# Performance work log

Measured on AMD Instinct MI355X. Metric: run time of the kernel, lower is better.

## Reference

```python
import jax, jax.numpy as jnp
import numpy as np

ROPE_THETA = 10000.0


def _rotate_half(x):
    # interleaved rotation: out[..., 2i] = -x[..., 2i+1], out[..., 2i+1] = x[..., 2i]
    x_even = x[..., ::2]
    x_odd = x[..., 1::2]
    return jnp.stack([-x_odd, x_even], axis=-1).reshape(x.shape)


def _rope_cos_sin(N, D, dtype):
    inv_freq = 1.0 / (ROPE_THETA ** (jnp.arange(0, D, 2, dtype=jnp.float32) / D))  # [D/2]
    angles = jnp.arange(N, dtype=jnp.float32)[:, None] * inv_freq[None, :]          # [N, D/2]
    angles = jnp.repeat(angles, 2, axis=-1)                                          # [N, D]
    cos = jnp.cos(angles).astype(dtype)[None, :, None, :]  # [1, N, 1, D]
    sin = jnp.sin(angles).astype(dtype)[None, :, None, :]
    return cos, sin


def setup_inputs() -> dict:
    key = jax.random.key(0)
    kq, kk, kv, km = jax.random.split(key, 4)
    B, N, H, D = 16, 1024, 8, 64
    xq = jax.random.normal(kq, (B, N, H, D), dtype=jnp.float32)
    xk = jax.random.normal(kk, (B, N, H, D), dtype=jnp.float32)
    xv = jax.random.normal(kv, (B, N, H, D), dtype=jnp.float32)
    vis_mask = jax.random.bernoulli(km, 0.8, (B, N))  # bool visibility mask per batch
    return {"xq": xq, "xk": xk, "xv": xv, "vis_mask": vis_mask}


def reference(xq, xk, xv, vis_mask):
    B, N, H, D = xq.shape
    sm_scale = 1.0 / np.sqrt(D).astype(np.float32)

    # RoPE (interleaved) on q and k
    cos, sin = _rope_cos_sin(N, D, xq.dtype)
    q = xq * cos + _rotate_half(xq) * sin
    k = xk * cos + _rotate_half(xk) * sin

    # masked full attention: scores [B, H, N, N]
    scores = jnp.einsum("bnhd,bmhd->bhnm", q, k) * sm_scale
    attn_mask = (vis_mask[:, None, :, None] & vis_mask[:, None, None, :])  # [B,1,N,N]
    scores = jnp.where(attn_mask, scores, -jnp.inf)
    p = jax.nn.softmax(scores, axis=-1)
    p = jnp.nan_to_num(p, nan=0.0)  # fully-masked rows -> zeros (matches fallback)
    out = jnp.einsum("bhnm,bmhd->bnhd", p, xv)
    return out
```

## Files before the change

### kernel.cpp

```cpp
#include <hip/hip_runtime.h>
#include <hip/hip_bf16.h>
#include <stdint.h>

#define Bb 16
#define Nn 1024
#define Hh 8
#define Dd 64

typedef unsigned short u16;
typedef float f32x4 __attribute__((ext_vector_type(4)));
typedef short short8 __attribute__((ext_vector_type(8)));

union U4S8 { uint4 u; short8 s; };
union BF2U { __hip_bfloat162 h; uint32_t u; };

__device__ __forceinline__ uint32_t f2bf(float f){
  union{float f;uint32_t i;} v; v.f=f;
  return (v.i + 0x7fffu + ((v.i>>16)&1u))>>16;
}

__device__ __forceinline__ f32x4 mfma16(short8 a, short8 b, f32x4 c){
  return __builtin_amdgcn_mfma_f32_16x16x32_bf16(a,b,c,0,0,0);
}

typedef __attribute__((address_space(3))) uint32_t lds_u32;
typedef const __attribute__((address_space(1))) uint32_t glb_u32;
__device__ __forceinline__ void gl_lds16(const u16* g, u16* l){
  __builtin_amdgcn_global_load_lds((glb_u32*)g, (lds_u32*)l, 16, 0, 0);
}

#define ROPE_K 0.41524101186092030f
#define QS 0.18033688011112042f
#define NEGBIG -1.0e30f

__global__ __launch_bounds__(256) void prepass_kernel(
    const float* __restrict__ xk, const float* __restrict__ xv,
    u16* __restrict__ Kf, u16* __restrict__ Vf)
{
  const int tid = threadIdx.x;
  const int bid = blockIdx.x;
  const int nt = bid & 15, h = (bid>>4)&7, b = bid>>7;
  const size_t bh = (size_t)b*Hh + h;
  const size_t tile = (bh<<4) + nt;

  {
    int r = tid>>2, c = (tid&3)<<4;
    int n = (nt<<6) + r;
    const float4* g = (const float4*)(xk + ((((size_t)b*Nn + n)*Hh + h)<<6) + c);
    float4 a0=g[0],a1=g[1],a2=g[2],a3=g[3];
    float xx[16] = {a0.x,a0.y,a0.z,a0.w, a1.x,a1.y,a1.z,a1.w,
                    a2.x,a2.y,a2.z,a2.w, a3.x,a3.y,a3.z,a3.w};
    uint32_t w[8];
    #pragma unroll
    for (int j=0;j<8;++j){
      int i = (c>>1)+j;
      float inv = exp2f(-(float)i * ROPE_K);
      float ang = (float)n * inv;
      float sn, cs; sincosf(ang, &sn, &cs);
      float x0 = xx[2*j], x1 = xx[2*j+1];
      float q0 = x0*cs - x1*sn;
      float q1 = x1*cs + x0*sn;
      w[j] = f2bf(q0) | (f2bf(q1)<<16);
    }
    int kb = r>>4, l15 = r&15;
    int half = c>>5, qd = (c>>3)&3;
    u16* base = Kf + (tile<<12);
    int dest0 = (kb<<10) + (half<<9) + (qd<<7) + (l15<<3);
    *(uint4*)(base + dest0)       = make_uint4(w[0],w[1],w[2],w[3]);
    *(uint4*)(base + dest0 + 128) = make_uint4(w[4],w[5],w[6],w[7]);
  }

  {
    int k = tid&63, ds = (tid>>6)<<4;
    int n = (nt<<6) + k;
    int slot = (k&1) | (((k>>4)&3)<<1) | (((k>>2)&3)<<3) | (((k>>1)&1)<<5);
    int half = slot>>5, qd = (slot>>3)&3, j = slot&7;
    const float4* g = (const float4*)(xv + ((((size_t)b*Nn + n)*Hh + h)<<6) + ds);
    float4 a0=g[0],a1=g[1],a2=g[2],a3=g[3];
    float vv[16] = {a0.x,a0.y,a0.z,a0.w, a1.x,a1.y,a1.z,a1.w,
                    a2.x,a2.y,a2.z,a2.w, a3.x,a3.y,a3.z,a3.w};
    u16* base = Vf + (tile<<12);
    #pragma unroll
    for (int jj=0;jj<16;++jj){
      int d = ds + jj;
      int s = d>>4, l15v = d&15;
      base[(s<<10) + (half<<9) + (qd<<7) + (l15v<<3) + j] = (u16)f2bf(vv[jj]);
    }
  }
}

__global__ __launch_bounds__(256,2) void attn8_kernel(
    const float* __restrict__ xq, const u16* __restrict__ Kf,
    const u16* __restrict__ Vf, const int* __restrict__ vis,
    float* __restrict__ out)
{
  __shared__ u16 KV[2][2][4096];

  const int tid  = threadIdx.x;
  const int lane = tid & 63;
  const int wave = tid >> 6;
  const int l15  = lane & 15;
  const int quad = lane >> 4;

  const int bid = blockIdx.x;
  const int xcd = bid & 7;
  const int i   = bid >> 3;
  const int bh_ = (xcd<<4) | (i>>2);
  const int qt  = i & 3;
  const int h   = bh_ & 7;
  const int b   = bh_ >> 3;
  const size_t bh = (size_t)bh_;
  const int qbase = qt<<8;

  const int* visb = vis + b*Nn;
  const u16* Kfb = Kf + (bh<<16);
  const u16* Vfb = Vf + (bh<<16);

  short8 qa[4][2];
  #pragma unroll
  for (int mb=0; mb<4; ++mb){
    int n = qbase + (wave<<6) + (mb<<4) + l15;
    const float* src = xq + ((((size_t)b*Nn + n)*Hh + h)<<6);
    #pragma unroll
    for (int half=0; half<2; ++half){
      int d0 = (half<<5) + (quad<<3);
      const float4* g = (const float4*)(src + d0);
      float4 u0 = g[0], u1 = g[1];
      float xx[8] = {u0.x,u0.y,u0.z,u0.w, u1.x,u1.y,u1.z,u1.w};
      uint32_t w[4];
      #pragma unroll
      for (int j=0;j<4;++j){
        int i2 = (d0>>1) + j;
        float inv = exp2f(-(float)i2 * ROPE_K);
        float ang = (float)n * inv;
        float sn, cs; sincosf(ang, &sn, &cs);
        float x0 = xx[2*j], x1 = xx[2*j+1];
        float q0 = (x0*cs - x1*sn)*QS;
        float q1 = (x1*cs + x0*sn)*QS;
        w[j] = f2bf(q0) | (f2bf(q1)<<16);
      }
      U4S8 t; t.u = make_uint4(w[0],w[1],w[2],w[3]);
      qa[mb][half] = t.s;
    }
  }

  U4S8 ones_u; ones_u.u = make_uint4(0x3F803F80u,0x3F803F80u,0x3F803F80u,0x3F803F80u);
  const short8 ones = ones_u.s;

  f32x4 acc[4][4];
  f32x4 l_acc[4];
  #pragma unroll
  for (int mb=0;mb<4;++mb){
    l_acc[mb] = (f32x4){0.f,0.f,0.f,0.f};
    #pragma unroll
    for (int s=0;s<4;++s) acc[mb][s] = (f32x4){0.f,0.f,0.f,0.f};
  }

  const int t8 = tid<<3;

  gl_lds16(Kfb + t8,        &KV[0][0][t8]);
  gl_lds16(Kfb + 2048 + t8, &KV[0][0][2048 + t8]);
  gl_lds16(Vfb + t8,        &KV[0][1][t8]);
  gl_lds16(Vfb + 2048 + t8, &KV[0][1][2048 + t8]);
  __syncthreads();

  for (int kt=0; kt<16; ++kt){
    const int cur = kt & 1;
    if (kt < 15){
      const u16* kg = Kfb + ((kt+1)<<12);
      const u16* vg = Vfb + ((kt+1)<<12);
      gl_lds16(kg + t8,        &KV[cur^1][0][t8]);
      gl_lds16(kg + 2048 + t8, &KV[cur^1][0][2048 + t8]);
      gl_lds16(vg + t8,        &KV[cur^1][1][t8]);
      gl_lds16(vg + 2048 + t8, &KV[cur^1][1][2048 + t8]);
    }

    uint32_t pk[4][2][4];
    #pragma unroll
    for (int kb=0;kb<4;++kb){
      short8 kf0 = *(const short8*)&KV[cur][0][(kb<<10) + (lane<<3)];
      short8 kf1 = *(const short8*)&KV[cur][0][(kb<<10) + 512 + (lane<<3)];
      int4 vi = *(const int4*)&visb[(kt<<6)+(kb<<4)+(quad<<2)];
      f32x4 bias;
      bias.x = vi.x ? 0.f : NEGBIG;
      bias.y = vi.y ? 0.f : NEGBIG;
      bias.z = vi.z ? 0.f : NEGBIG;
      bias.w = vi.w ? 0.f : NEGBIG;
      #pragma unroll
      for (int mb=0;mb<4;++mb){
        f32x4 t = mfma16(kf0, qa[mb][0], bias);
        t = mfma16(kf1, qa[mb][1], t);
        float p0 = __builtin_amdgcn_exp2f(t.x);
        float p1 = __builtin_amdgcn_exp2f(t.y);
        float p2 = __builtin_amdgcn_exp2f(t.z);
        float p3 = __builtin_amdgcn_exp2f(t.w);
        BF2U e0; e0.h = __float22bfloat162_rn(make_float2(p0,p1));
        BF2U e1; e1.h = __float22bfloat162_rn(make_float2(p2,p3));
        pk[kb][0][mb] = e0.u;
        pk[kb][1][mb] = e1.u;
      }
    }

    short8 pa[4][2];
    #pragma unroll
    for (int mb=0;mb<4;++mb){
      U4S8 a0; a0.u = make_uint4(pk[0][0][mb], pk[1][0][mb], pk[2][0][mb], pk[3][0][mb]);
      U4S8 a1; a1.u = make_uint4(pk[0][1][mb], pk[1][1][mb], pk[2][1][mb], pk[3][1][mb]);
      pa[mb][0] = a0.s; pa[mb][1] = a1.s;
    }

    #pragma unroll
    for (int mb=0;mb<4;++mb){
      l_acc[mb] = mfma16(pa[mb][0], ones, l_acc[mb]);
      l_acc[mb] = mfma16(pa[mb][1], ones, l_acc[mb]);
    }
    #pragma unroll
    for (int s=0;s<4;++s){
      short8 vb0 = *(const short8*)&KV[cur][1][(s<<10) + (lane<<3)];
      short8 vb1 = *(const short8*)&KV[cur][1][(s<<10) + 512 + (lane<<3)];
      #pragma unroll
      for (int mb=0;mb<4;++mb){
        acc[mb][s] = mfma16(pa[mb][0], vb0, acc[mb][s]);
        acc[mb][s] = mfma16(pa[mb][1], vb1, acc[mb][s]);
      }
    }

    __syncthreads();
  }

  #pragma unroll
  for (int mb=0;mb<4;++mb){
    int4 qvi = *(const int4*)&visb[qbase + (wave<<6) + (mb<<4) + (quad<<2)];
    int qv[4] = {qvi.x, qvi.y, qvi.z, qvi.w};
    #pragma unroll
    for (int rr=0;rr<4;++rr){
      float lq = l_acc[mb][rr];
      float invl = (qv[rr] != 0 && lq > 0.f) ? 1.f/lq : 0.f;
      int qrow = qbase + (wave<<6) + (mb<<4) + (quad<<2) + rr;
      float* ob = out + ((((size_t)b*Nn + qrow)*Hh + h)<<6);
      #pragma unroll
      for (int s=0;s<4;++s)
        ob[(s<<4)+l15] = acc[mb][s][rr]*invl;
    }
  }
}

__device__ __forceinline__ void stage_rope_row_fb(const float* __restrict__ src,
                                                  u16 (*dst)[72],
                                                  int n_global, int sr, int d0)
{
  const float4* g = (const float4*)src;
  float4 a0 = g[0], a1 = g[1], a2 = g[2], a3 = g[3];
  float xx[16] = {a0.x,a0.y,a0.z,a0.w, a1.x,a1.y,a1.z,a1.w,
                  a2.x,a2.y,a2.z,a2.w, a3.x,a3.y,a3.z,a3.w};
  uint32_t w[8];
  #pragma unroll
  for (int j=0;j<8;++j){
    int i = (d0>>1)+j;
    float inv = exp2f(-(float)i * ROPE_K);
    float ang = (float)n_global * inv;
    float sn, cs; sincosf(ang, &sn, &cs);
    float x0 = xx[2*j], x1 = xx[2*j+1];
    float q0 = x0*cs - x1*sn;
    float q1 = x1*cs + x0*sn;
    w[j] = f2bf(q0) | (f2bf(q1)<<16);
  }
  *(uint4*)&dst[sr][d0]   = make_uint4(w[0],w[1],w[2],w[3]);
  *(uint4*)&dst[sr][d0+8] = make_uint4(w[4],w[5],w[6],w[7]);
}

__global__ __launch_bounds__(256,2) void attn_fallback(
    const float* __restrict__ xq, const float* __restrict__ xk,
    const float* __restrict__ xv, const int* __restrict__ vis,
    float* __restrict__ out)
{
  __shared__ u16 Qs[64][72];
  __shared__ u16 Ks[64][72];
  __shared__ u16 Vt[64][72];
  __shared__ u16 Ps[4][16][72];
  __shared__ float viss[64];

  const int tid  = threadIdx.x;
  const int wave = tid >> 6;
  const int lane = tid & 63;
  const int l15  = lane & 15;
  const int quad = lane >> 4;

  const int bid = blockIdx.x;
  const int qt = bid & 15;
  const int h  = (bid >> 4) & 7;
  const int b  = bid >> 7;

  const int sr = tid >> 2;
  const int d0 = (tid & 3) << 4;

  {
    int ng = (qt<<6) + sr;
    const float* src = xq + ((((size_t)b*Nn + ng)*Hh + h)<<6) + d0;
    stage_rope_row_fb(src, Qs, ng, sr, d0);
  }
  __syncthreads();

  short8 qa0 = *(const short8*)&Qs[(wave<<4)+l15][quad<<3];
  short8 qa1 = *(const short8*)&Qs[(wave<<4)+l15][(quad<<3)+32];

  f32x4 acc[4];
  #pragma unroll
  for (int s=0;s<4;++s) acc[s] = (f32x4){0.f,0.f,0.f,0.f};
  float m_r[4], l_r[4];
  #pragma unroll
  for (int rr=0;rr<4;++rr){ m_r[rr] = -1e30f; l_r[rr] = 0.f; }

  for (int kt=0; kt<16; ++kt){
    __syncthreads();
    {
      int ng = (kt<<6) + sr;
      const float* src = xk + ((((size_t)b*Nn + ng)*Hh + h)<<6) + d0;
      stage_rope_row_fb(src, Ks, ng, sr, d0);
    }
    {
      int ng = (kt<<6) + sr;
      const float4* g = (const float4*)(xv + ((((size_t)b*Nn + ng)*Hh + h)<<6) + d0);
      float4 a0 = g[0], a1 = g[1], a2 = g[2], a3 = g[3];
      float vv16[16] = {a0.x,a0.y,a0.z,a0.w, a1.x,a1.y,a1.z,a1.w,
                        a2.x,a2.y,a2.z,a2.w, a3.x,a3.y,a3.z,a3.w};
      #pragma unroll
      for (int j=0;j<16;++j) Vt[d0+j][sr] = (u16)f2bf(vv16[j]);
    }
    if (tid < 64) viss[tid] = (vis[b*Nn + (kt<<6) + tid] != 0) ? 1.f : 0.f;
    __syncthreads();

    f32x4 s4[4];
    #pragma unroll
    for (int n=0;n<4;++n){
      short8 kb0 = *(const short8*)&Ks[(n<<4)+l15][quad<<3];
      short8 kb1 = *(const short8*)&Ks[(n<<4)+l15][(quad<<3)+32];
      f32x4 t = (f32x4){0.f,0.f,0.f,0.f};
      t = mfma16(qa0, kb0, t);
      t = mfma16(qa1, kb1, t);
      s4[n] = t;
    }
    float vv[4];
    #pragma unroll
    for (int n=0;n<4;++n) vv[n] = viss[(n<<4)+l15];

    float p[4][4];
    #pragma unroll
    for (int rr=0; rr<4; ++rr){
      float sc[4];
      #pragma unroll
      for (int n=0;n<4;++n) sc[n] = (vv[n] > 0.f) ? s4[n][rr]*0.125f : -1e30f;
      float tm = fmaxf(fmaxf(sc[0],sc[1]), fmaxf(sc[2],sc[3]));
      tm = fmaxf(tm, __shfl_xor(tm,1));
      tm = fmaxf(tm, __shfl_xor(tm,2));
      tm = fmaxf(tm, __shfl_xor(tm,4));
      tm = fmaxf(tm, __shfl_xor(tm,8));
      float mnew  = fmaxf(m_r[rr], tm);
      float alpha = __expf(m_r[rr] - mnew);
      m_r[rr] = mnew;
      float psum = 0.f;
      #pragma unroll
      for (int n=0;n<4;++n){
        float pv = (vv[n] > 0.f) ? __expf(sc[n] - mnew) : 0.f;
        p[n][rr] = pv; psum += pv;
      }
      l_r[rr] = l_r[rr]*alpha + psum;
      #pragma unroll
      for (int s=0;s<4;++s) acc[s][rr] *= alpha;
    }

    #pragma unroll
    for (int n=0;n<4;++n)
      #pragma unroll
      for (int rr=0;rr<4;++rr)
        Ps[wave][(quad<<2)+rr][(n<<4)+l15] = (u16)f2bf(p[n][rr]);
    asm volatile("s_waitcnt lgkmcnt(0)" ::: "memory");
    short8 pa0 = *(const short8*)&Ps[wave][l15][quad<<3];
    short8 pa1 = *(const short8*)&Ps[wave][l15][(quad<<3)+32];

    #pragma unroll
    for (int s=0;s<4;++s){
      short8 vb0 = *(const short8*)&Vt[(s<<4)+l15][quad<<3];
      short8 vb1 = *(const short8*)&Vt[(s<<4)+l15][(quad<<3)+32];
      acc[s] = mfma16(pa0, vb0, acc[s]);
      acc[s] = mfma16(pa1, vb1, acc[s]);
    }
  }

  #pragma unroll
  for (int rr=0;rr<4;++rr){
    float t = l_r[rr];
    t += __shfl_xor(t,1); t += __shfl_xor(t,2);
    t += __shfl_xor(t,4); t += __shfl_xor(t,8);
    int row = (qt<<6) + (wave<<4) + (quad<<2) + rr;
    int qv  = vis[b*Nn + row];
    float invl = (qv != 0 && t > 0.f) ? 1.f/t : 0.f;
    size_t obase = (((size_t)b*Nn + row)*Hh + h) << 6;
    #pragma unroll
    for (int s=0;s<4;++s)
      out[obase + (s<<4) + l15] = acc[s][rr]*invl;
  }
}

extern "C" void kernel_launch(void* const* d_in, const int* in_sizes, int n_in,
                              void* d_out, int out_size, void* d_ws, size_t ws_size,
                              hipStream_t stream)
{
  const float* xq = (const float*)d_in[0];
  const float* xk = (const float*)d_in[1];
  const float* xv = (const float*)d_in[2];
  const int* vis  = (const int*)d_in[3];
  float* out = (float*)d_out;

  const size_t kv_elems = (size_t)Bb*Hh*Nn*Dd;
  const size_t kv_bytes = kv_elems*sizeof(u16);
  const size_t need_kv  = 2*kv_bytes;

  if (d_ws != nullptr && ws_size >= need_kv){
    u16* Kf = (u16*)d_ws;
    u16* Vf = Kf + kv_elems;
    prepass_kernel<<<dim3(Bb*Hh*(Nn/64)), dim3(256), 0, stream>>>(xk, xv, Kf, Vf);
    attn8_kernel<<<dim3(Bb*Hh*(Nn/256)), dim3(256), 0, stream>>>(xq, Kf, Vf, vis, out);
  } else {
    attn_fallback<<<dim3(Bb*Hh*(Nn/64)), dim3(256), 0, stream>>>(xq, xk, xv, vis, out);
  }
}
```

Measured before the change: 190.1 us.

## Halve attention query tile, raise occupancy, precompute RoPE table and LDS mask bias

The attention kernel now gives each block 128 query rows instead of 256, so each wave handles 32 rows. This doubles the grid to 1024 blocks and raises the launch-bounds occupancy hint from 2 to 4 blocks per CU. A separate kernel precomputes a cos/sin RoPE table in the workspace, and both the prepass and attention kernels read it instead of calling sincosf. The visibility mask is turned into a float bias array in LDS once per block rather than re-read from global memory every key tile. In exchange, K/V tiles are loaded twice as often per query row, and there is an extra kernel launch plus a larger workspace requirement.

```diff
diff --git a/kernel.cpp b/kernel.cpp
--- a/kernel.cpp
+++ b/kernel.cpp
@@ -33,9 +33,20 @@
 #define QS 0.18033688011112042f
 #define NEGBIG -1.0e30f
 
+__global__ __launch_bounds__(256) void rope_table_kernel(float2* __restrict__ tab)
+{
+  int id = blockIdx.x*256 + threadIdx.x;
+  int i = id >> 10, n = id & 1023;
+  float inv = exp2f(-(float)i * ROPE_K);
+  float sn, cs; sincosf((float)n * inv, &sn, &cs);
+  tab[id] = make_float2(cs, sn);
+}
+
+template<int USE_TAB>
 __global__ __launch_bounds__(256) void prepass_kernel(
     const float* __restrict__ xk, const float* __restrict__ xv,
-    u16* __restrict__ Kf, u16* __restrict__ Vf)
+    u16* __restrict__ Kf, u16* __restrict__ Vf,
+    const float2* __restrict__ tab)
 {
   const int tid = threadIdx.x;
   const int bid = blockIdx.x;
@@ -53,10 +64,14 @@
     uint32_t w[8];
     #pragma unroll
     for (int j=0;j<8;++j){
-      int i = (c>>1)+j;
-      float inv = exp2f(-(float)i * ROPE_K);
-      float ang = (float)n * inv;
-      float sn, cs; sincosf(ang, &sn, &cs);
+      int ii = (c>>1)+j;
+      float cs, sn;
+      if (USE_TAB){
+        float2 t = tab[(ii<<10)+n]; cs = t.x; sn = t.y;
+      } else {
+        float inv = exp2f(-(float)ii * ROPE_K);
+        sincosf((float)n * inv, &sn, &cs);
+      }
       float x0 = xx[2*j], x1 = xx[2*j+1];
       float q0 = x0*cs - x1*sn;
       float q1 = x1*cs + x0*sn;
@@ -89,12 +104,14 @@
   }
 }
 
-__global__ __launch_bounds__(256,2) void attn8_kernel(
+template<int USE_TAB>
+__global__ __launch_bounds__(256,4) void attn8_kernel(
     const float* __restrict__ xq, const u16* __restrict__ Kf,
     const u16* __restrict__ Vf, const int* __restrict__ vis,
-    float* __restrict__ out)
+    const float2* __restrict__ tab, float* __restrict__ out)
 {
   __shared__ u16 KV[2][2][4096];
+  __shared__ float biasS[Nn];
 
   const int tid  = threadIdx.x;
   const int lane = tid & 63;
@@ -104,22 +121,32 @@
 
   const int bid = blockIdx.x;
   const int xcd = bid & 7;
-  const int i   = bid >> 3;
-  const int bh_ = (xcd<<4) | (i>>2);
-  const int qt  = i & 3;
+  const int ix  = bid >> 3;
+  const int bh_ = (xcd<<4) | (ix>>3);
+  const int qt  = ix & 7;
   const int h   = bh_ & 7;
   const int b   = bh_ >> 3;
   const size_t bh = (size_t)bh_;
-  const int qbase = qt<<8;
+  const int qbase = qt<<7;
 
   const int* visb = vis + b*Nn;
   const u16* Kfb = Kf + (bh<<16);
   const u16* Vfb = Vf + (bh<<16);
 
-  short8 qa[4][2];
-  #pragma unroll
-  for (int mb=0; mb<4; ++mb){
-    int n = qbase + (wave<<6) + (mb<<4) + l15;
+  {
+    int4 vi = *(const int4*)&visb[tid<<2];
+    float4 bs;
+    bs.x = vi.x ? 0.f : NEGBIG;
+    bs.y = vi.y ? 0.f : NEGBIG;
+    bs.z = vi.z ? 0.f : NEGBIG;
+    bs.w = vi.w ? 0.f : NEGBIG;
+    *(float4*)&biasS[tid<<2] = bs;
+  }
+
+  short8 qa[2][2];
+  #pragma unroll
+  for (int mb=0; mb<2; ++mb){
+    int n = qbase + (wave<<5) + (mb<<4) + l15;
     const float* src = xq + ((((size_t)b*Nn + n)*Hh + h)<<6);
     #pragma unroll
     for (int half=0; half<2; ++half){
@@ -131,9 +158,13 @@
       #pragma unroll
       for (int j=0;j<4;++j){
         int i2 = (d0>>1) + j;
-        float inv = exp2f(-(float)i2 * ROPE_K);
-        float ang = (float)n * inv;
-        float sn, cs; sincosf(ang, &sn, &cs);
+        float cs, sn;
+        if (USE_TAB){
+          float2 t = tab[(i2<<10)+n]; cs = t.x; sn = t.y;
+        } else {
+          float inv = exp2f(-(float)i2 * ROPE_K);
+          sincosf((float)n * inv, &sn, &cs);
+        }
         float x0 = xx[2*j], x1 = xx[2*j+1];
         float q0 = (x0*cs - x1*sn)*QS;
         float q1 = (x1*cs + x0*sn)*QS;
@@ -147,10 +178,10 @@
   U4S8 ones_u; ones_u.u = make_uint4(0x3F803F80u,0x3F803F80u,0x3F803F80u,0x3F803F80u);
   const short8 ones = ones_u.s;
 
-  f32x4 acc[4][4];
-  f32x4 l_acc[4];
-  #pragma unroll
-  for (int mb=0;mb<4;++mb){
+  f32x4 acc[2][4];
+  f32x4 l_acc[2];
+  #pragma unroll
+  for (int mb=0;mb<2;++mb){
     l_acc[mb] = (f32x4){0.f,0.f,0.f,0.f};
     #pragma unroll
     for (int s=0;s<4;++s) acc[mb][s] = (f32x4){0.f,0.f,0.f,0.f};
@@ -175,19 +206,14 @@
       gl_lds16(vg + 2048 + t8, &KV[cur^1][1][2048 + t8]);
     }
 
-    uint32_t pk[4][2][4];
+    uint32_t pk[4][2][2];
     #pragma unroll
     for (int kb=0;kb<4;++kb){
       short8 kf0 = *(const short8*)&KV[cur][0][(kb<<10) + (lane<<3)];
       short8 kf1 = *(const short8*)&KV[cur][0][(kb<<10) + 512 + (lane<<3)];
-      int4 vi = *(const int4*)&visb[(kt<<6)+(kb<<4)+(quad<<2)];
-      f32x4 bias;
-      bias.x = vi.x ? 0.f : NEGBIG;
-      bias.y = vi.y ? 0.f : NEGBIG;
-      bias.z = vi.z ? 0.f : NEGBIG;
-      bias.w = vi.w ? 0.f : NEGBIG;
-      #pragma unroll
-      for (int mb=0;mb<4;++mb){
+      f32x4 bias = *(const f32x4*)&biasS[(kt<<6)+(kb<<4)+(quad<<2)];
+      #pragma unroll
+      for (int mb=0;mb<2;++mb){
         f32x4 t = mfma16(kf0, qa[mb][0], bias);
         t = mfma16(kf1, qa[mb][1], t);
         float p0 = __builtin_amdgcn_exp2f(t.x);
@@ -201,16 +227,16 @@
       }
     }
 
-    short8 pa[4][2];
-    #pragma unroll
-    for (int mb=0;mb<4;++mb){
+    short8 pa[2][2];
+    #pragma unroll
+    for (int mb=0;mb<2;++mb){
       U4S8 a0; a0.u = make_uint4(pk[0][0][mb], pk[1][0][mb], pk[2][0][mb], pk[3][0][mb]);
       U4S8 a1; a1.u = make_uint4(pk[0][1][mb], pk[1][1][mb], pk[2][1][mb], pk[3][1][mb]);
       pa[mb][0] = a0.s; pa[mb][1] = a1.s;
     }
 
     #pragma unroll
-    for (int mb=0;mb<4;++mb){
+    for (int mb=0;mb<2;++mb){
       l_acc[mb] = mfma16(pa[mb][0], ones, l_acc[mb]);
       l_acc[mb] = mfma16(pa[mb][1], ones, l_acc[mb]);
     }
@@ -219,7 +245,7 @@
       short8 vb0 = *(const short8*)&KV[cur][1][(s<<10) + (lane<<3)];
       short8 vb1 = *(const short8*)&KV[cur][1][(s<<10) + 512 + (lane<<3)];
       #pragma unroll
-      for (int mb=0;mb<4;++mb){
+      for (int mb=0;mb<2;++mb){
         acc[mb][s] = mfma16(pa[mb][0], vb0, acc[mb][s]);
         acc[mb][s] = mfma16(pa[mb][1], vb1, acc[mb][s]);
       }
@@ -229,14 +255,12 @@
   }
 
   #pragma unroll
-  for (int mb=0;mb<4;++mb){
-    int4 qvi = *(const int4*)&visb[qbase + (wave<<6) + (mb<<4) + (quad<<2)];
-    int qv[4] = {qvi.x, qvi.y, qvi.z, qvi.w};
+  for (int mb=0;mb<2;++mb){
     #pragma unroll
     for (int rr=0;rr<4;++rr){
+      int qrow = qbase + (wave<<5) + (mb<<4) + (quad<<2) + rr;
       float lq = l_acc[mb][rr];
-      float invl = (qv[rr] != 0 && lq > 0.f) ? 1.f/lq : 0.f;
-      int qrow = qbase + (wave<<6) + (mb<<4) + (quad<<2) + rr;
+      float invl = (biasS[qrow] == 0.f && lq > 0.f) ? 1.f/lq : 0.f;
       float* ob = out + ((((size_t)b*Nn + qrow)*Hh + h)<<6);
       #pragma unroll
       for (int s=0;s<4;++s)
@@ -415,12 +439,20 @@
   const size_t kv_elems = (size_t)Bb*Hh*Nn*Dd;
   const size_t kv_bytes = kv_elems*sizeof(u16);
   const size_t need_kv  = 2*kv_bytes;
-
-  if (d_ws != nullptr && ws_size >= need_kv){
+  const size_t tab_bytes = (size_t)32*1024*sizeof(float2);
+
+  if (d_ws != nullptr && ws_size >= need_kv + tab_bytes){
     u16* Kf = (u16*)d_ws;
     u16* Vf = Kf + kv_elems;
-    prepass_kernel<<<dim3(Bb*Hh*(Nn/64)), dim3(256), 0, stream>>>(xk, xv, Kf, Vf);
-    attn8_kernel<<<dim3(Bb*Hh*(Nn/256)), dim3(256), 0, stream>>>(xq, Kf, Vf, vis, out);
+    float2* tab = (float2*)((char*)d_ws + need_kv);
+    rope_table_kernel<<<dim3(128), dim3(256), 0, stream>>>(tab);
+    prepass_kernel<1><<<dim3(Bb*Hh*(Nn/64)), dim3(256), 0, stream>>>(xk, xv, Kf, Vf, tab);
+    attn8_kernel<1><<<dim3(Bb*Hh*(Nn/128)), dim3(256), 0, stream>>>(xq, Kf, Vf, vis, tab, out);
+  } else if (d_ws != nullptr && ws_size >= need_kv){
+    u16* Kf = (u16*)d_ws;
+    u16* Vf = Kf + kv_elems;
+    prepass_kernel<0><<<dim3(Bb*Hh*(Nn/64)), dim3(256), 0, stream>>>(xk, xv, Kf, Vf, nullptr);
+    attn8_kernel<0><<<dim3(Bb*Hh*(Nn/128)), dim3(256), 0, stream>>>(xq, Kf, Vf, vis, nullptr, out);
   } else {
     attn_fallback<<<dim3(Bb*Hh*(Nn/64)), dim3(256), 0, stream>>>(xq, xk, xv, vis, out);
   }
```

New measurement: 189.6 us. No clear change (-0.2%).
